# Kernel optimization log

Hardware: AMD Instinct MI355X
Metric: run time of the kernel (lower is better)

## Reference

```python
import jax, jax.numpy as jnp
import numpy as np

H = 16        # num attention heads
KVH = 4       # num key/value heads
D = 128       # head dim
WIN = 1024    # sliding window (in packed per-state positions)
THETA = 10000.0
NUM_STATES = 8


def rotate_half(x):
    half = x.shape[-1] // 2
    return jnp.concatenate([-x[..., half:], x[..., :half]], axis=-1)


def setup_inputs() -> dict:
    key = jax.random.key(0)
    ks = jax.random.split(key, 6)
    B, L, HID = 2, 2048, 2048
    s = 0.02
    hidden_states = jax.random.normal(ks[0], (B, L, HID), jnp.float32)
    Wq = jax.random.normal(ks[1], (H * D, HID), jnp.float32) * s
    Wk = jax.random.normal(ks[2], (KVH * D, HID), jnp.float32) * s
    Wv = jax.random.normal(ks[3], (KVH * D, HID), jnp.float32) * s
    Wo = jax.random.normal(ks[4], (HID, H * D), jnp.float32) * s
    sid = jax.random.randint(ks[5], (B, L), 0, NUM_STATES).astype(jnp.int64)
    position_ids = jnp.tile(jnp.arange(L, dtype=jnp.int64)[None, :], (B, 1))
    return dict(hidden_states=hidden_states, Wq=Wq, Wk=Wk, Wv=Wv, Wo=Wo,
                sid=sid, position_ids=position_ids)


def reference(hidden_states, Wq, Wk, Wv, Wo, sid, position_ids):
    B, L, HID = hidden_states.shape
    # projections (Linear without bias: x @ W.T)
    q = (hidden_states @ Wq.T).reshape(B, L, H, D)
    k = (hidden_states @ Wk.T).reshape(B, L, KVH, D)
    v = (hidden_states @ Wv.T).reshape(B, L, KVH, D)
    # rotary embedding
    inv_freq = 1.0 / (THETA ** (jnp.arange(0, D, 2, dtype=jnp.float32) / D))
    freqs = position_ids.astype(jnp.float32)[:, :, None] * inv_freq[None, None, :]  # [B,L,D/2]
    emb = jnp.concatenate([freqs, freqs], axis=-1)                                  # [B,L,D]
    cos = jnp.cos(emb)[:, :, None, :].astype(hidden_states.dtype)
    sin = jnp.sin(emb)[:, :, None, :].astype(hidden_states.dtype)
    q = q * cos + rotate_half(q) * sin
    k = k * cos + rotate_half(k) * sin
    # GQA: repeat kv heads (repeat_interleave along head dim)
    n_rep = H // KVH
    k = jnp.repeat(k, n_rep, axis=2)  # [B,L,H,D]
    v = jnp.repeat(v, n_rep, axis=2)
    # BoSs mask: attend within same state id, causal, sliding window over
    # packed-per-state rank distance (equivalent to the varlen packing path)
    same = sid[:, :, None] == sid[:, None, :]                  # [B,L,L]
    tril = jnp.tril(jnp.ones((L, L), dtype=bool))[None]        # [1,L,L]
    rank = jnp.sum(same & tril, axis=-1) - 1                   # [B,L] rank within own state
    win_ok = (rank[:, :, None] - rank[:, None, :]) <= WIN
    mask = same & tril & win_ok                                # [B,L,L]
    scale = D ** -0.5
    scores = jnp.einsum('bqhd,bkhd->bhqk', q, k) * scale       # [B,H,L,L]
    scores = jnp.where(mask[:, None, :, :], scores, jnp.finfo(scores.dtype).min)
    attn = jax.nn.softmax(scores, axis=-1)
    o = jnp.einsum('bhqk,bkhd->bqhd', attn, v).reshape(B, L, H * D)
    return o @ Wo.T
```

## Files before the change

### kernel.cpp

```cpp
#include <hip/hip_runtime.h>
#include <hip/hip_bf16.h>

#define H_ 16
#define KVH_ 4
#define D_ 128
#define L_ 2048
#define B_ 2
#define HID_ 2048
#define WIN_ 1024
#define NS_ 8
#define QKV_N 3072

typedef __attribute__((ext_vector_type(8))) short short8;
typedef __attribute__((ext_vector_type(4))) float floatx4;

__device__ inline float bf16_to_f(unsigned short u) {
    union { unsigned int i; float f; } c; c.i = ((unsigned int)u) << 16; return c.f;
}
__device__ inline unsigned short f_to_bf16(float f) {
    __hip_bfloat16 h = __float2bfloat16(f);
    return *(unsigned short*)&h;
}

__device__ inline int world_is_bf16(const unsigned short* hs_u) {
    int lane = threadIdx.x & 63;
    unsigned short u = hs_u[(lane & 31) * 2];
    int e = (u >> 7) & 0xFF;
    unsigned long long bad = __ballot(e > 130);
    return bad == 0ULL;
}
__device__ inline int pid_stride(const int* pids) { return (pids[1] == 0) ? 2 : 1; }

__global__ __launch_bounds__(256) void convert_all(const void* __restrict__ hs,
                                                   const void* __restrict__ Wq,
                                                   const void* __restrict__ Wk,
                                                   const void* __restrict__ Wv,
                                                   const void* __restrict__ Wo,
                                                   unsigned short* __restrict__ c_hs,
                                                   unsigned short* __restrict__ c_Wq,
                                                   unsigned short* __restrict__ c_Wk,
                                                   unsigned short* __restrict__ c_Wv,
                                                   unsigned short* __restrict__ c_Wo) {
    int isbf = world_is_bf16((const unsigned short*)hs);
    const int N0 = (B_ * L_ * HID_) / 4;
    const int N1 = (HID_ * HID_) / 4;
    const int N2 = (KVH_ * D_ * HID_) / 4;
    const int N3 = N2;
    const int N4 = N1;
    const int total = N0 + N1 + N2 + N3 + N4;
    for (int i = blockIdx.x * 256 + threadIdx.x; i < total; i += gridDim.x * 256) {
        int j = i;
        const void* src; unsigned short* dst;
        if (j < N0)              { src = hs; dst = c_hs; }
        else if ((j -= N0) < N1) { src = Wq; dst = c_Wq; }
        else if ((j -= N1) < N2) { src = Wk; dst = c_Wk; }
        else if ((j -= N2) < N3) { src = Wv; dst = c_Wv; }
        else                     { j -= N3; src = Wo; dst = c_Wo; }
        if (isbf) {
            ((ushort4*)dst)[j] = ((const ushort4*)src)[j];
        } else {
            float4 f = ((const float4*)src)[j];
            ushort4 o4;
            o4.x = f_to_bf16(f.x); o4.y = f_to_bf16(f.y);
            o4.z = f_to_bf16(f.z); o4.w = f_to_bf16(f.w);
            ((ushort4*)dst)[j] = o4;
        }
    }
}

__global__ __launch_bounds__(256) void scan_kernel(const int* __restrict__ sid,
                                                   const int* __restrict__ pids,
                                                   int* __restrict__ rank,
                                                   int* __restrict__ poslist,
                                                   int* __restrict__ counts) {
    int stride = pid_stride(pids);
    int b = blockIdx.x;
    int t = threadIdx.x;
    __shared__ int cnt[256][NS_];
    __shared__ int pre[256][NS_];
    const int* s = sid + (size_t)b * L_ * stride;
    int myid[8];
#pragma unroll
    for (int i = 0; i < 8; i++) myid[i] = s[(t * 8 + i) * stride];
#pragma unroll
    for (int st = 0; st < NS_; st++) cnt[t][st] = 0;
#pragma unroll
    for (int i = 0; i < 8; i++) cnt[t][myid[i]]++;
    __syncthreads();
    for (int off = 1; off < 256; off <<= 1) {
        int add[NS_];
        if (t >= off)
#pragma unroll
            for (int st = 0; st < NS_; st++) add[st] = cnt[t - off][st];
        __syncthreads();
        if (t >= off)
#pragma unroll
            for (int st = 0; st < NS_; st++) cnt[t][st] += add[st];
        __syncthreads();
    }
#pragma unroll
    for (int st = 0; st < NS_; st++) pre[t][st] = t ? cnt[t - 1][st] : 0;
    if (t == 255)
#pragma unroll
        for (int st = 0; st < NS_; st++) counts[b * NS_ + st] = cnt[255][st];
    __syncthreads();
#pragma unroll
    for (int i = 0; i < 8; i++) {
        int sd = myid[i];
        int r = pre[t][sd]++;
        int pos = t * 8 + i;
        rank[b * L_ + pos] = r;
        poslist[((size_t)b * NS_ + sd) * L_ + r] = pos;
    }
}

#define STAGE(gptr, ldsdst)                                                     \
    __builtin_amdgcn_global_load_lds(                                           \
        (const __attribute__((address_space(1))) unsigned int*)(gptr),          \
        (__attribute__((address_space(3))) unsigned int*)(ldsdst), 16, 0, 0)

#define READ_A(QM)                                                              \
    _Pragma("unroll")                                                           \
    for (int mt = 0; mt < 4; ++mt)                                              \
        _Pragma("unroll")                                                       \
        for (int kk = 0; kk < 2; ++kk)                                          \
            af[mt][kk] = *(const short8*)&Ab[(arow + (QM) * 128 + mt * 16) * 64 \
                                             + (((kk << 2) | quad) ^ axor) * 8]

#define READ_B(QN)                                                              \
    _Pragma("unroll")                                                           \
    for (int nt = 0; nt < 2; ++nt)                                              \
        _Pragma("unroll")                                                       \
        for (int kk = 0; kk < 2; ++kk)                                          \
            bf[QN][nt][kk] = *(const short8*)&Bb[(brow_r + (QN) * 128 + nt * 16) * 64 \
                                                 + (((kk << 2) | quad) ^ axor) * 8]

#define MFMA_Q(QM, QN)                                                          \
    __builtin_amdgcn_s_setprio(1);                                              \
    _Pragma("unroll")                                                           \
    for (int kk = 0; kk < 2; ++kk)                                              \
        _Pragma("unroll")                                                       \
        for (int mt = 0; mt < 4; ++mt)                                          \
            _Pragma("unroll")                                                   \
            for (int nt = 0; nt < 2; ++nt)                                      \
                acc[(QM) * 4 + mt][(QN) * 2 + nt] =                             \
                    __builtin_amdgcn_mfma_f32_16x16x32_bf16(                    \
                        af[mt][kk], bf[QN][nt][kk],                             \
                        acc[(QM) * 4 + mt][(QN) * 2 + nt], 0, 0, 0);            \
    __builtin_amdgcn_s_setprio(0)

#define PH_BAR() do { __builtin_amdgcn_s_barrier();                             \
                      asm volatile("" ::: "memory"); } while (0)

__global__ __launch_bounds__(512, 2) void gemm256(const unsigned short* __restrict__ A,
                                                  const unsigned short* __restrict__ B0,
                                                  const unsigned short* __restrict__ B1,
                                                  const unsigned short* __restrict__ B2,
                                                  void* __restrict__ C,
                                                  int M, int N, int K,
                                                  int nb1, int nb2,
                                                  const unsigned short* __restrict__ hs_probe,
                                                  int c_mode) {
    __shared__ unsigned short As[2][16384];
    __shared__ unsigned short Bs[2][16384];
    int tid = threadIdx.x;
    int wave = tid >> 6, lane = tid & 63;
    int quad = lane >> 4, l16 = lane & 15;
    int wr = wave >> 2, wc = wave & 3;
    int bn_t = blockIdx.x;
    int bm = blockIdx.y * 256, bn = bn_t * 256;

    const unsigned short* Bseg;
    int brow0;
    if (bn_t < nb1)      { Bseg = B0; brow0 = bn; }
    else if (bn_t < nb2) { Bseg = B1; brow0 = bn - nb1 * 256; }
    else                 { Bseg = B2; brow0 = bn - nb2 * 256; }

    int sub = tid >> 3;
    int slot = tid & 7;
    unsigned int a_off[4], b_off[4];
#pragma unroll
    for (int i = 0; i < 4; ++i) {
        int lr = i * 64 + sub;
        int swz = slot ^ (lr & 7);
        int grow = (lr & 63) + ((lr >> 6) & 1) * 128 + (lr >> 7) * 64;
        a_off[i] = (unsigned int)((bm + grow) * K + swz * 8);
        int wcb = (lr >> 5) & 3, qnb = lr >> 7, rr = lr & 31;
        int brow = wcb * 64 + qnb * 32 + rr;
        b_off[i] = (unsigned int)((brow0 + brow) * K + swz * 8);
    }

    const int arow = wr * 64 + l16;
    const int brow_r = wc * 32 + l16;
    const int axor = l16 & 7;

    floatx4 acc[8][4] = {};
    short8 af[4][2];
    short8 bf[2][2][2];
    const int KT = K >> 6;

    STAGE(A + a_off[0], &As[0][0 * 4096 + tid * 8]);
    STAGE(A + a_off[1], &As[0][1 * 4096 + tid * 8]);
    STAGE(Bseg + b_off[0], &Bs[0][0 * 4096 + tid * 8]);
    STAGE(Bseg + b_off[1], &Bs[0][1 * 4096 + tid * 8]);
    STAGE(A + a_off[2], &As[0][2 * 4096 + tid * 8]);
    STAGE(A + a_off[3], &As[0][3 * 4096 + tid * 8]);
    STAGE(Bseg + b_off[2], &Bs[0][2 * 4096 + tid * 8]);
    STAGE(Bseg + b_off[3], &Bs[0][3 * 4096 + tid * 8]);

    for (int t = 0; t < KT; ++t) {
        const unsigned short* Ab = As[t & 1];
        const unsigned short* Bb = Bs[t & 1];
        unsigned short* AsN = As[(t & 1) ^ 1];
        unsigned short* BsN = Bs[(t & 1) ^ 1];
        int tn = (t + 1 < KT) ? t + 1 : t;
        unsigned int kel = (unsigned int)tn * 64;

        asm volatile("s_waitcnt vmcnt(4)" ::: "memory");
        PH_BAR();
        STAGE(A + a_off[0] + kel, &AsN[0 * 4096 + tid * 8]);
        STAGE(A + a_off[1] + kel, &AsN[1 * 4096 + tid * 8]);
        READ_A(0);
        READ_B(0);
        MFMA_Q(0, 0);

        asm volatile("s_waitcnt vmcnt(2)" ::: "memory");
        PH_BAR();
        STAGE(Bseg + b_off[0] + kel, &BsN[0 * 4096 + tid * 8]);
        STAGE(Bseg + b_off[1] + kel, &BsN[1 * 4096 + tid * 8]);
        READ_B(1);
        MFMA_Q(0, 1);

        PH_BAR();
        STAGE(A + a_off[2] + kel, &AsN[2 * 4096 + tid * 8]);
        STAGE(A + a_off[3] + kel, &AsN[3 * 4096 + tid * 8]);
        READ_A(1);
        MFMA_Q(1, 1);

        PH_BAR();
        STAGE(Bseg + b_off[2] + kel, &BsN[2 * 4096 + tid * 8]);
        STAGE(Bseg + b_off[3] + kel, &BsN[3 * 4096 + tid * 8]);
        MFMA_Q(1, 0);
    }
    asm volatile("s_waitcnt vmcnt(0)" ::: "memory");

    int cf32 = c_mode ? !world_is_bf16(hs_probe) : 0;
#pragma unroll
    for (int a = 0; a < 8; ++a)
#pragma unroll
        for (int g = 0; g < 4; ++g)
#pragma unroll
            for (int r = 0; r < 4; ++r) {
                int row = bm + wr * 128 + (a >> 2) * 64 + (a & 3) * 16 + quad * 4 + r;
                int col = bn + wc * 64 + (g >> 1) * 32 + (g & 1) * 16 + l16;
                size_t idx = (size_t)row * N + col;
                if (cf32) ((float*)C)[idx] = acc[a][g][r];
                else      ((unsigned short*)C)[idx] = f_to_bf16(acc[a][g][r]);
            }
}

__global__ __launch_bounds__(256) void rope_kernel(unsigned short* __restrict__ qkv,
                                                   const int* __restrict__ pos_ids) {
    int stride = pid_stride(pos_ids);
    int idx = blockIdx.x * 256 + threadIdx.x;
    int i = idx & 63;
    int tmp = idx >> 6;
    int head = tmp % 20;
    int bl = tmp / 20;
    if (bl >= B_ * L_) return;
    float posf = (float)pos_ids[bl * stride];
    float inv = exp2f(-(float)i * (2.0f / 128.0f) * 13.287712379549449f);
    float ang = posf * inv;
    float c = cosf(ang), sn = sinf(ang);
    unsigned short* p = qkv + (size_t)bl * QKV_N +
                        ((head < H_) ? head * D_ : 2048 + (head - H_) * D_);
    float x0 = bf16_to_f(p[i]), x1 = bf16_to_f(p[i + 64]);
    p[i]      = f_to_bf16(x0 * c - x1 * sn);
    p[i + 64] = f_to_bf16(x1 * c + x0 * sn);
}

__global__ __launch_bounds__(256, 4) void attn_mfma(const unsigned short* __restrict__ qkv,
                                                    const int* __restrict__ counts,
                                                    const int* __restrict__ poslist,
                                                    unsigned short* __restrict__ o) {
    int qt  = blockIdx.x & 127;
    int kvh = (blockIdx.x >> 7) & 3;
    int s   = (blockIdx.x >> 9) & 7;
    int b   = blockIdx.x >> 12;
    int n = counts[b * NS_ + s];
    if (qt * 16 >= n) return;
    const int* plist = poslist + ((size_t)b * NS_ + s) * L_;

    __shared__ short Ksh[32][136];
    __shared__ short Vsh[128][40];
    __shared__ short Psh[4][16][40];
    __shared__ int posq[16];

    int tid = threadIdx.x;
    int wave = tid >> 6, lane = tid & 63;
    int quad = lane >> 4, l16 = lane & 15;
    int h = kvh * 4 + wave;
    const float scale = 0.08838834764831845f;

    if (tid < 16) posq[tid] = plist[min(qt * 16 + tid, n - 1)];
    __syncthreads();

    short8 qf[4];
    {
        const unsigned short* gq =
            qkv + ((size_t)(b << 11) + posq[l16]) * QKV_N + h * D_;
#pragma unroll
        for (int kk = 0; kk < 4; kk++)
            qf[kk] = *(const short8*)(gq + kk * 32 + quad * 8);
    }

    float m_r[4], l_r[4];
    floatx4 Ov[8];
#pragma unroll
    for (int r4 = 0; r4 < 4; r4++) { m_r[r4] = -1e30f; l_r[r4] = 0.f; }
#pragma unroll
    for (int nt = 0; nt < 8; nt++) Ov[nt] = (floatx4){0.f, 0.f, 0.f, 0.f};

    int c0 = max(0, (qt * 16 - WIN_) >> 5);
    int nch = ((qt * 16 + 15) >> 5) + 1;

    int r = tid >> 3, seg = tid & 7;
    int vc = r ^ ((seg & 3) << 3);
    short8 kr0, kr1, vr0, vr1;
    {
        int kpos = plist[min(c0 * 32 + r, n - 1)];
        size_t base = ((size_t)(b << 11) + kpos) * QKV_N + 2048 + kvh * D_ + seg * 16;
        kr0 = *(const short8*)(qkv + base);
        kr1 = *(const short8*)(qkv + base + 8);
        vr0 = *(const short8*)(qkv + base + 512);
        vr1 = *(const short8*)(qkv + base + 520);
    }

    for (int c = c0; c < nch; c++) {
        *(short8*)&Ksh[r][seg * 16]     = kr0;
        *(short8*)&Ksh[r][seg * 16 + 8] = kr1;
#pragma unroll
        for (int e = 0; e < 8; e++) Vsh[seg * 16 + e][vc] = vr0[e];
#pragma unroll
        for (int e = 0; e < 8; e++) Vsh[seg * 16 + 8 + e][vc] = vr1[e];
        __syncthreads();

        if (c + 1 < nch) {
            int kpos = plist[min((c + 1) * 32 + r, n - 1)];
            size_t base = ((size_t)(b << 11) + kpos) * QKV_N + 2048 + kvh * D_ + seg * 16;
            kr0 = *(const short8*)(qkv + base);
            kr1 = *(const short8*)(qkv + base + 8);
            vr0 = *(const short8*)(qkv + base + 512);
            vr1 = *(const short8*)(qkv + base + 520);
        }

        floatx4 s0 = (floatx4){0.f, 0.f, 0.f, 0.f};
        floatx4 s1 = (floatx4){0.f, 0.f, 0.f, 0.f};
#pragma unroll
        for (int kk = 0; kk < 4; kk++) {
            short8 kfa = *(const short8*)&Ksh[l16][kk * 32 + quad * 8];
            s0 = __builtin_amdgcn_mfma_f32_16x16x32_bf16(qf[kk], kfa, s0, 0, 0, 0);
        }
#pragma unroll
        for (int kk = 0; kk < 4; kk++) {
            short8 kfb = *(const short8*)&Ksh[16 + l16][kk * 32 + quad * 8];
            s1 = __builtin_amdgcn_mfma_f32_16x16x32_bf16(qf[kk], kfb, s1, 0, 0, 0);
        }

        int kr0i = c * 32 + l16, kr1i = kr0i + 16;
        float x0[4], x1[4], rmax[4];
#pragma unroll
        for (int r4 = 0; r4 < 4; r4++) {
            int qr = qt * 16 + quad * 4 + r4;
            bool mk0 = (kr0i <= qr) && (kr0i >= qr - WIN_);
            bool mk1 = (kr1i <= qr) && (kr1i >= qr - WIN_);
            x0[r4] = mk0 ? s0[r4] * scale : -1e30f;
            x1[r4] = mk1 ? s1[r4] * scale : -1e30f;
            rmax[r4] = fmaxf(x0[r4], x1[r4]);
        }
#pragma unroll
        for (int st = 1; st <= 8; st <<= 1)
#pragma unroll
            for (int r4 = 0; r4 < 4; r4++)
                rmax[r4] = fmaxf(rmax[r4], __shfl_xor(rmax[r4], st, 64));
        float al[4], psum[4];
#pragma unroll
        for (int r4 = 0; r4 < 4; r4++) {
            float nm = fmaxf(m_r[r4], rmax[r4]);
            al[r4] = __expf(m_r[r4] - nm);
            m_r[r4] = nm;
            x0[r4] = (x0[r4] > -1e29f) ? __expf(x0[r4] - nm) : 0.f;
            x1[r4] = (x1[r4] > -1e29f) ? __expf(x1[r4] - nm) : 0.f;
            psum[r4] = x0[r4] + x1[r4];
        }
#pragma unroll
        for (int st = 1; st <= 8; st <<= 1)
#pragma unroll
            for (int r4 = 0; r4 < 4; r4++)
                psum[r4] += __shfl_xor(psum[r4], st, 64);
#pragma unroll
        for (int r4 = 0; r4 < 4; r4++) l_r[r4] = l_r[r4] * al[r4] + psum[r4];
#pragma unroll
        for (int nt = 0; nt < 8; nt++)
#pragma unroll
            for (int r4 = 0; r4 < 4; r4++) Ov[nt][r4] *= al[r4];

#pragma unroll
        for (int r4 = 0; r4 < 4; r4++) {
            Psh[wave][quad * 4 + r4][l16]      = (short)f_to_bf16(x0[r4]);
            Psh[wave][quad * 4 + r4][16 + l16] = (short)f_to_bf16(x1[r4]);
        }
        short8 pf = *(const short8*)&Psh[wave][l16][quad * 8];

#pragma unroll
        for (int nt = 0; nt < 8; nt++) {
            short8 vf = *(const short8*)&Vsh[nt * 16 + l16][(quad ^ (nt & 3)) * 8];
            Ov[nt] = __builtin_amdgcn_mfma_f32_16x16x32_bf16(pf, vf, Ov[nt], 0, 0, 0);
        }
        __syncthreads();
    }

    float inv_r[4];
    int pos_r[4], qvalid[4];
#pragma unroll
    for (int r4 = 0; r4 < 4; r4++) {
        int qr = qt * 16 + quad * 4 + r4;
        qvalid[r4] = (qr < n);
        inv_r[r4] = 1.f / l_r[r4];
        pos_r[r4] = posq[quad * 4 + r4];
    }
#pragma unroll
    for (int nt = 0; nt < 8; nt++)
#pragma unroll
        for (int r4 = 0; r4 < 4; r4++)
            if (qvalid[r4])
                o[(((size_t)(b << 11) + pos_r[r4]) * H_ + h) * D_ + nt * 16 + l16] =
                    f_to_bf16(Ov[nt][r4] * inv_r[r4]);
}

extern "C" void kernel_launch(void* const* d_in, const int* in_sizes, int n_in,
                              void* d_out, int out_size, void* d_ws, size_t ws_size,
                              hipStream_t stream) {
    const void* hs = d_in[0];
    const void* Wq = d_in[1];
    const void* Wk = d_in[2];
    const void* Wv = d_in[3];
    const void* Wo = d_in[4];
    const int* sid  = (const int*)d_in[5];
    const int* pids = (const int*)d_in[6];

    const int M = B_ * L_;
    char* w = (char*)d_ws;
    unsigned short* qkv  = (unsigned short*)(w + 256);
    unsigned short* o_b  = (unsigned short*)(w + 25166080);
    unsigned short* c_hs = (unsigned short*)(w + 41943296);
    unsigned short* c_Wq = (unsigned short*)(w + 58720512);
    unsigned short* c_Wk = (unsigned short*)(w + 67109120);
    unsigned short* c_Wv = (unsigned short*)(w + 69206272);
    unsigned short* c_Wo = (unsigned short*)(w + 71303424);
    int* rank            = (int*)(w + 79692032);
    int* plist           = (int*)(w + 79708416);
    int* counts          = (int*)(w + 79839488);

    const unsigned short* hs_probe = (const unsigned short*)hs;

    convert_all<<<2048, 256, 0, stream>>>(hs, Wq, Wk, Wv, Wo,
                                          c_hs, c_Wq, c_Wk, c_Wv, c_Wo);

    scan_kernel<<<B_, 256, 0, stream>>>(sid, pids, rank, plist, counts);

    gemm256<<<dim3(QKV_N / 256, M / 256), 512, 0, stream>>>(
        c_hs, c_Wq, c_Wk, c_Wv, qkv, M, QKV_N, HID_, 8, 10, hs_probe, 0);

    int rope_threads = M * (H_ + KVH_) * 64;
    rope_kernel<<<(rope_threads + 255) / 256, 256, 0, stream>>>(qkv, pids);

    attn_mfma<<<B_ * NS_ * KVH_ * (L_ / 16), 256, 0, stream>>>(qkv, counts, plist, o_b);

    gemm256<<<dim3(HID_ / 256, M / 256), 512, 0, stream>>>(
        o_b, c_Wo, c_Wo, c_Wo, d_out, M, HID_, HID_, 1 << 30, 1 << 30, hs_probe, 1);
}
```

Baseline: 347.1 us.

## Restructure 256x256 GEMM main loop into k-split halves with fewer barriers

Reorganizes the bf16 GEMM inner loop from four quadrant phases with a barrier each into four k-half/m-half phases: B tiles are staged first, A rows are laid out contiguously, and each phase reads A/B fragments, issues the next prefetch, waits on lgkmcnt(0) and runs 16 MFMAs. Only two barriers remain per k-step, and launch bounds move from 2 blocks per CU to 1, which allows more registers per thread. The aim is to cut barrier stalls and register pressure from holding both k-halves of fragments, at the cost of less inter-block latency hiding and a tighter LDS reuse window.

```diff
diff --git a/kernel.cpp b/kernel.cpp
--- a/kernel.cpp
+++ b/kernel.cpp
@@ -119,40 +119,38 @@
         (const __attribute__((address_space(1))) unsigned int*)(gptr),          \
         (__attribute__((address_space(3))) unsigned int*)(ldsdst), 16, 0, 0)
 
-#define READ_A(QM)                                                              \
+#define READ_A(MH, KK)                                                          \
+    _Pragma("unroll")                                                           \
+    for (int mt = 0; mt < 4; ++mt)                                              \
+        af[mt] = *(const short8*)&Ab[(arow + (MH) * 64 + mt * 16) * 64          \
+                                     + ((((KK) << 2) | quad) ^ axor) * 8]
+
+#define READ_B(KK)                                                              \
+    _Pragma("unroll")                                                           \
+    for (int nt = 0; nt < 4; ++nt)                                              \
+        bf[nt] = *(const short8*)&Bb[(brr + nt * 16) * 64                       \
+                                     + ((((KK) << 2) | quad) ^ axor) * 8]
+
+#define MFMA_H(MH)                                                              \
+    __builtin_amdgcn_s_setprio(1);                                              \
     _Pragma("unroll")                                                           \
     for (int mt = 0; mt < 4; ++mt)                                              \
         _Pragma("unroll")                                                       \
-        for (int kk = 0; kk < 2; ++kk)                                          \
-            af[mt][kk] = *(const short8*)&Ab[(arow + (QM) * 128 + mt * 16) * 64 \
-                                             + (((kk << 2) | quad) ^ axor) * 8]
-
-#define READ_B(QN)                                                              \
-    _Pragma("unroll")                                                           \
-    for (int nt = 0; nt < 2; ++nt)                                              \
-        _Pragma("unroll")                                                       \
-        for (int kk = 0; kk < 2; ++kk)                                          \
-            bf[QN][nt][kk] = *(const short8*)&Bb[(brow_r + (QN) * 128 + nt * 16) * 64 \
-                                                 + (((kk << 2) | quad) ^ axor) * 8]
-
-#define MFMA_Q(QM, QN)                                                          \
-    __builtin_amdgcn_s_setprio(1);                                              \
-    _Pragma("unroll")                                                           \
-    for (int kk = 0; kk < 2; ++kk)                                              \
-        _Pragma("unroll")                                                       \
-        for (int mt = 0; mt < 4; ++mt)                                          \
-            _Pragma("unroll")                                                   \
-            for (int nt = 0; nt < 2; ++nt)                                      \
-                acc[(QM) * 4 + mt][(QN) * 2 + nt] =                             \
-                    __builtin_amdgcn_mfma_f32_16x16x32_bf16(                    \
-                        af[mt][kk], bf[QN][nt][kk],                             \
-                        acc[(QM) * 4 + mt][(QN) * 2 + nt], 0, 0, 0);            \
+        for (int nt = 0; nt < 4; ++nt)                                          \
+            acc[(MH) * 4 + mt][nt] = __builtin_amdgcn_mfma_f32_16x16x32_bf16(   \
+                af[mt], bf[nt], acc[(MH) * 4 + mt][nt], 0, 0, 0);               \
     __builtin_amdgcn_s_setprio(0)
 
-#define PH_BAR() do { __builtin_amdgcn_s_barrier();                             \
-                      asm volatile("" ::: "memory"); } while (0)
-
-__global__ __launch_bounds__(512, 2) void gemm256(const unsigned short* __restrict__ A,
+#define LGKM0_PIN() do {                                                        \
+    asm volatile("s_waitcnt lgkmcnt(0)" ::: "memory");                          \
+    __builtin_amdgcn_sched_barrier(0); } while (0)
+
+#define VM2_BAR() do {                                                          \
+    asm volatile("s_waitcnt vmcnt(2)" ::: "memory");                            \
+    __builtin_amdgcn_s_barrier();                                               \
+    asm volatile("" ::: "memory"); } while (0)
+
+__global__ __launch_bounds__(512, 1) void gemm256(const unsigned short* __restrict__ A,
                                                   const unsigned short* __restrict__ B0,
                                                   const unsigned short* __restrict__ B1,
                                                   const unsigned short* __restrict__ B2,
@@ -176,37 +174,31 @@
     else if (bn_t < nb2) { Bseg = B1; brow0 = bn - nb1 * 256; }
     else                 { Bseg = B2; brow0 = bn - nb2 * 256; }
 
-    int sub = tid >> 3;
-    int slot = tid & 7;
+    int sub = tid >> 3, slot = tid & 7;
+    int swz = slot ^ (sub & 7);
     unsigned int a_off[4], b_off[4];
 #pragma unroll
-    for (int i = 0; i < 4; ++i) {
-        int lr = i * 64 + sub;
-        int swz = slot ^ (lr & 7);
-        int grow = (lr & 63) + ((lr >> 6) & 1) * 128 + (lr >> 7) * 64;
-        a_off[i] = (unsigned int)((bm + grow) * K + swz * 8);
-        int wcb = (lr >> 5) & 3, qnb = lr >> 7, rr = lr & 31;
-        int brow = wcb * 64 + qnb * 32 + rr;
-        b_off[i] = (unsigned int)((brow0 + brow) * K + swz * 8);
-    }
-
-    const int arow = wr * 64 + l16;
-    const int brow_r = wc * 32 + l16;
+    for (int c = 0; c < 4; ++c) {
+        a_off[c] = (unsigned int)((bm + c * 64 + sub) * K + swz * 8);
+        b_off[c] = (unsigned int)((brow0 + c * 64 + sub) * K + swz * 8);
+    }
+
+    const int arow = wr * 128 + l16;
+    const int brr  = wc * 64 + l16;
     const int axor = l16 & 7;
 
     floatx4 acc[8][4] = {};
-    short8 af[4][2];
-    short8 bf[2][2][2];
+    short8 af[4], bf[4];
     const int KT = K >> 6;
 
-    STAGE(A + a_off[0], &As[0][0 * 4096 + tid * 8]);
-    STAGE(A + a_off[1], &As[0][1 * 4096 + tid * 8]);
     STAGE(Bseg + b_off[0], &Bs[0][0 * 4096 + tid * 8]);
     STAGE(Bseg + b_off[1], &Bs[0][1 * 4096 + tid * 8]);
-    STAGE(A + a_off[2], &As[0][2 * 4096 + tid * 8]);
-    STAGE(A + a_off[3], &As[0][3 * 4096 + tid * 8]);
     STAGE(Bseg + b_off[2], &Bs[0][2 * 4096 + tid * 8]);
     STAGE(Bseg + b_off[3], &Bs[0][3 * 4096 + tid * 8]);
+    STAGE(A + a_off[0], &As[0][0 * 4096 + tid * 8]);
+    STAGE(A + a_off[2], &As[0][2 * 4096 + tid * 8]);
+    STAGE(A + a_off[1], &As[0][1 * 4096 + tid * 8]);
+    STAGE(A + a_off[3], &As[0][3 * 4096 + tid * 8]);
 
     for (int t = 0; t < KT; ++t) {
         const unsigned short* Ab = As[t & 1];
@@ -216,31 +208,33 @@
         int tn = (t + 1 < KT) ? t + 1 : t;
         unsigned int kel = (unsigned int)tn * 64;
 
-        asm volatile("s_waitcnt vmcnt(4)" ::: "memory");
-        PH_BAR();
-        STAGE(A + a_off[0] + kel, &AsN[0 * 4096 + tid * 8]);
-        STAGE(A + a_off[1] + kel, &AsN[1 * 4096 + tid * 8]);
-        READ_A(0);
+        VM2_BAR();
+        READ_A(0, 0);
         READ_B(0);
-        MFMA_Q(0, 0);
-
-        asm volatile("s_waitcnt vmcnt(2)" ::: "memory");
-        PH_BAR();
         STAGE(Bseg + b_off[0] + kel, &BsN[0 * 4096 + tid * 8]);
         STAGE(Bseg + b_off[1] + kel, &BsN[1 * 4096 + tid * 8]);
-        READ_B(1);
-        MFMA_Q(0, 1);
-
-        PH_BAR();
-        STAGE(A + a_off[2] + kel, &AsN[2 * 4096 + tid * 8]);
-        STAGE(A + a_off[3] + kel, &AsN[3 * 4096 + tid * 8]);
-        READ_A(1);
-        MFMA_Q(1, 1);
-
-        PH_BAR();
+        LGKM0_PIN();
+        MFMA_H(0);
+
+        VM2_BAR();
+        READ_A(1, 0);
         STAGE(Bseg + b_off[2] + kel, &BsN[2 * 4096 + tid * 8]);
         STAGE(Bseg + b_off[3] + kel, &BsN[3 * 4096 + tid * 8]);
-        MFMA_Q(1, 0);
+        LGKM0_PIN();
+        MFMA_H(1);
+
+        READ_A(0, 1);
+        READ_B(1);
+        STAGE(A + a_off[0] + kel, &AsN[0 * 4096 + tid * 8]);
+        STAGE(A + a_off[2] + kel, &AsN[2 * 4096 + tid * 8]);
+        LGKM0_PIN();
+        MFMA_H(0);
+
+        READ_A(1, 1);
+        STAGE(A + a_off[1] + kel, &AsN[1 * 4096 + tid * 8]);
+        STAGE(A + a_off[3] + kel, &AsN[3 * 4096 + tid * 8]);
+        LGKM0_PIN();
+        MFMA_H(1);
     }
     asm volatile("s_waitcnt vmcnt(0)" ::: "memory");
 
@@ -252,7 +246,7 @@
 #pragma unroll
             for (int r = 0; r < 4; ++r) {
                 int row = bm + wr * 128 + (a >> 2) * 64 + (a & 3) * 16 + quad * 4 + r;
-                int col = bn + wc * 64 + (g >> 1) * 32 + (g & 1) * 16 + l16;
+                int col = bn + wc * 64 + g * 16 + l16;
                 size_t idx = (size_t)row * N + col;
                 if (cf32) ((float*)C)[idx] = acc[a][g][r];
                 else      ((unsigned short*)C)[idx] = f_to_bf16(acc[a][g][r]);
```

Measured after the change: 313.8 us. -9.6%, faster.
